# Kernel optimization log

Measured on AMD Instinct MI355X. Metric: run time of the kernel, lower is better.

## Reference

```python
import jax, jax.numpy as jnp
import numpy as np
from jax import lax

TABLE_SIZE = 1024   # LSH table buckets
R = 2.5             # hash bucket width r
U = 0.83            # ALSH norm rescale bound
M = 9               # appended ALSH dims; M // (K*K) = 1 extra channel
K = 3               # kernel spatial size
PAD = 1


def _P(kflat, m):
    # L2-ALSH preprocessing: rescale so max row norm == U, append ||x||^{2^i}, i=1..m
    norms = jnp.linalg.norm(kflat, axis=1)
    x = kflat * (U / jnp.max(norms))
    p = jnp.sum(x * x, axis=1)  # ||x||^2
    powers = [p]
    for _ in range(m - 1):
        powers.append(powers[-1] ** 2)
    return jnp.concatenate([x, jnp.stack(powers, axis=1)], axis=1)  # [O, D+m]


def _conv(x, w):
    return lax.conv_general_dilated(
        x, w, window_strides=(1, 1), padding=[(PAD, PAD), (PAD, PAD)],
        dimension_numbers=("NCHW", "OIHW", "NCHW"))


def setup_inputs() -> dict:
    key = jax.random.key(0)
    k1, k2, k3, k4 = jax.random.split(key, 4)
    inp = jax.random.normal(k1, (16, 128, 64, 64), jnp.float32)
    kernels = jax.random.normal(k2, (256, 128, 3, 3), jnp.float32) * 0.05
    d = 128 + M // (K * K)  # 129
    a = jax.random.normal(k3, (d * K * K,), jnp.float32)  # 1161
    b = jax.random.uniform(k4, (1,), jnp.float32) * R
    return {"input": inp, "kernels": kernels, "a": a, "b": b}


def reference(input, kernels, a, b):
    O, C, kh, kw = kernels.shape
    B, _, H, W = input.shape
    extra_ch = M // (kh * kw)
    d = C + extra_ch

    # ---- init_table: hash every kernel row into a bucket ----
    kflat = kernels.reshape(O, -1)                       # [O, C*kh*kw]
    h = jnp.floor((_P(kflat, M) @ a + b[0]) / R)         # [O]
    bucket = jnp.abs(jnp.fmod(h.astype(jnp.int32), TABLE_SIZE))  # torch fmod+abs semantics

    # ---- vote: Q appends 0.5-filled channels, conv with hash vector as kernel ----
    input_Q = jnp.concatenate(
        [input, jnp.full((B, extra_ch, H, W), 0.5, input.dtype)], axis=1)
    dotted = _conv(input_Q, a.reshape(1, d, kh, kw))     # [B,1,H,W]
    votes = jnp.floor((dotted.reshape(-1) + b[0]) / R).astype(jnp.int32)
    vbucket = jnp.abs(jnp.fmod(votes, TABLE_SIZE))

    # ---- count_votes + argmax bucket ----
    count = jax.ops.segment_sum(jnp.ones(vbucket.shape, jnp.float32),
                                vbucket, num_segments=TABLE_SIZE)
    index = jnp.argmax(count)

    # ---- active set: kernels whose table bucket == winning bucket (mask form, jit-safe) ----
    mask = (bucket == index)                             # [O] bool
    active_kernels = kernels * mask[:, None, None, None].astype(kernels.dtype)

    # apply the active set (the conv this module feeds downstream)
    out = _conv(input, active_kernels)                   # [B,O,H,W]
    return out, index, mask
```

## Files before the change

kernel.cpp:

```cpp
#include <hip/hip_runtime.h>
#include <cmath>
#include <cstdint>

#define TSZ 1024
#define RDIV 2.5f
#define UCONST 0.83f

typedef __bf16 bf16x8 __attribute__((ext_vector_type(8)));
typedef float f32x4 __attribute__((ext_vector_type(4)));
typedef unsigned short ushortT;

__device__ __forceinline__ ushortT bf16r(float f) {
  union { float f; unsigned u; } x; x.f = f;
  unsigned r = (x.u + 0x7FFFu + ((x.u >> 16) & 1u)) >> 16;
  return (ushortT)r;
}

__device__ __forceinline__ void glds16(const void* g, void* l) {
  __builtin_amdgcn_global_load_lds(
      (const __attribute__((address_space(1))) unsigned int*)(g),
      (__attribute__((address_space(3))) unsigned int*)(l), 16, 0, 0);
}

__global__ __launch_bounds__(256) void k_cvtg(const float* __restrict__ in,
                                              const float* __restrict__ a,
                                              ushortT* __restrict__ nb,
                                              float* __restrict__ g) {
  __shared__ float tile2[64][129];
  __shared__ float gpart[4][9][64];
  const int bid = blockIdx.x;
  const int n = bid >> 6, y = bid & 63;
  const int t = threadIdx.x;

  {
    const int chs = t >> 4, l16 = t & 15;
    const float* basep = in + ((size_t)(n * 128) << 12) + (y << 6) + (l16 << 2);
#pragma unroll
    for (int i = 0; i < 8; ++i) {
      int ch = (i << 4) + chs;
      f32x4 v = *reinterpret_cast<const f32x4*>(basep + ((size_t)ch << 12));
#pragma unroll
      for (int u = 0; u < 4; ++u) tile2[(l16 << 2) + u][ch] = v[u];
    }
  }
  __syncthreads();

  {
    const int part = __builtin_amdgcn_readfirstlane(t >> 6);
    const int x = t & 63;
    float gacc[9];
#pragma unroll
    for (int tap = 0; tap < 9; ++tap) gacc[tap] = 0.f;
    const int c0 = part << 5;
#pragma unroll
    for (int i = 0; i < 32; ++i) {
      float v = tile2[x][c0 + i];
      const float* ap = a + (c0 + i) * 9;
#pragma unroll
      for (int tap = 0; tap < 9; ++tap) gacc[tap] += v * ap[tap];
    }
#pragma unroll
    for (int tap = 0; tap < 9; ++tap) gpart[part][tap][x] = gacc[tap];
  }
  __syncthreads();

  if (t < 64) {
    const int x = t;
#pragma unroll
    for (int tap = 0; tap < 9; ++tap) {
      float s = gpart[0][tap][x] + gpart[1][tap][x] + gpart[2][tap][x] + gpart[3][tap][x];
      g[tap * 65536 + (n << 12) + (y << 6) + x] = s;
    }
  }

  {
    const int x2 = t >> 2;
    ushortT* dst = nb + (((size_t)((n << 6) + y) << 6) + x2) * 128;
#pragma unroll
    for (int j = 0; j < 4; ++j) {
      int c0 = ((t & 3) << 3) + (j << 5);
      union { ushortT us[8]; uint4 v; } pk;
#pragma unroll
      for (int u = 0; u < 8; ++u) pk.us[u] = bf16r(tile2[x2][c0 + u]);
      *reinterpret_cast<uint4*>(dst + c0) = pk.v;
    }
  }
}

__global__ __launch_bounds__(256) void k_vote3(const float* __restrict__ g,
                                               const float* __restrict__ a,
                                               const float* __restrict__ bb,
                                               int* __restrict__ count) {
  __shared__ int hist[TSZ];
  const int t = threadIdx.x;
  for (int i = t; i < TSZ; i += 256) hist[i] = 0;
  __syncthreads();
  const int pix = blockIdx.x * 256 + t;
  const int n = pix >> 12, y = (pix >> 6) & 63, x = pix & 63;
  float acc = 0.f;
#pragma unroll
  for (int tap = 0; tap < 9; ++tap) {
    const int dy = tap / 3 - 1, dx = tap % 3 - 1;
    const int yy = y + dy, xx = x + dx;
    if ((unsigned)yy < 64u && (unsigned)xx < 64u)
      acc += g[tap * 65536 + (n << 12) + (yy << 6) + xx];
  }
  {
    const float* av = a + 1152;
#pragma unroll
    for (int ky = 0; ky < 3; ++ky) {
      int yy = y + ky - 1;
      if ((unsigned)yy >= 64u) continue;
#pragma unroll
      for (int kx = 0; kx < 3; ++kx) {
        int xx = x + kx - 1;
        if ((unsigned)xx >= 64u) continue;
        acc += 0.5f * av[ky * 3 + kx];
      }
    }
  }
  int v = (int)floorf((acc + bb[0]) / RDIV);
  int r = v % TSZ; if (r < 0) r = -r;
  atomicAdd(&hist[r], 1);
  __syncthreads();
  for (int i = t; i < TSZ; i += 256) {
    int h = hist[i];
    if (h) atomicAdd(&count[i], h);
  }
}

__global__ __launch_bounds__(256) void k_norm(const float* __restrict__ k,
                                              unsigned* __restrict__ scaleBits) {
  int o = blockIdx.x;
  const float* row = k + (size_t)o * 1152;
  float s = 0.f;
  for (int j = threadIdx.x; j < 1152; j += 256) { float v = row[j]; s += v * v; }
  __shared__ float red[256];
  red[threadIdx.x] = s; __syncthreads();
  for (int st = 128; st; st >>= 1) {
    if (threadIdx.x < st) red[threadIdx.x] += red[threadIdx.x + st];
    __syncthreads();
  }
  if (threadIdx.x == 0) atomicMax(scaleBits, __float_as_uint(red[0]));
}

__global__ __launch_bounds__(256) void k_hash(const float* __restrict__ k,
                                              const float* __restrict__ a,
                                              const float* __restrict__ b,
                                              const unsigned* __restrict__ scaleBits,
                                              int* __restrict__ bucket) {
  int o = blockIdx.x;
  float scale = UCONST / sqrtf(__uint_as_float(scaleBits[0]));
  const float* row = k + (size_t)o * 1152;
  float dot = 0.f, p = 0.f;
  for (int j = threadIdx.x; j < 1152; j += 256) {
    float x = row[j] * scale;
    dot += x * a[j];
    p += x * x;
  }
  __shared__ float rd[256], rp[256];
  rd[threadIdx.x] = dot; rp[threadIdx.x] = p; __syncthreads();
  for (int st = 128; st; st >>= 1) {
    if (threadIdx.x < st) { rd[threadIdx.x] += rd[threadIdx.x + st]; rp[threadIdx.x] += rp[threadIdx.x + st]; }
    __syncthreads();
  }
  if (threadIdx.x == 0) {
    float acc = rd[0];
    float pw = rp[0];
    for (int i = 0; i < 9; i++) { acc += pw * a[1152 + i]; pw = pw * pw; }
    acc += b[0];
    float h = floorf(acc / RDIV);
    int hi = (int)h;
    int r = hi % TSZ; if (r < 0) r = -r;
    bucket[o] = r;
  }
}

__global__ __launch_bounds__(1024) void k_argmax(const int* __restrict__ count,
                                                 const int* __restrict__ bucket,
                                                 int* __restrict__ maskI,
                                                 float* __restrict__ tail) {
  __shared__ int sc[1024];
  __shared__ int si[1024];
  int t = threadIdx.x;
  sc[t] = count[t]; si[t] = t; __syncthreads();
  for (int st = 512; st; st >>= 1) {
    if (t < st) {
      int c2 = sc[t + st], i2 = si[t + st];
      if (c2 > sc[t] || (c2 == sc[t] && i2 < si[t])) { sc[t] = c2; si[t] = i2; }
    }
    __syncthreads();
  }
  int idx = si[0];
  if (t == 0) tail[0] = (float)idx;
  if (t < 256) {
    int m = (bucket[t] == idx) ? 1 : 0;
    maskI[t] = m;
    tail[1 + t] = (float)m;
  }
}

__global__ __launch_bounds__(256) void k_wprep(const float* __restrict__ w,
                                               const int* __restrict__ maskI,
                                               ushortT* __restrict__ wb) {
  const int o = blockIdx.x;
  const float m = maskI[o] ? 1.f : 0.f;
  const float* wr = w + (size_t)o * 1152;
  ushortT* dst = wb + (size_t)o * 1152;
  for (int j = threadIdx.x; j < 1152; j += 256) {
    int r = j >> 7, c = j & 127;
    dst[j] = bf16r(wr[c * 9 + r] * m);
  }
}

__global__ __launch_bounds__(512, 2) void k_gemm3(const ushortT* __restrict__ nb,
                                                  const ushortT* __restrict__ wb,
                                                  const char* __restrict__ zp,
                                                  float* __restrict__ out) {
  __shared__ __align__(16) char smem[3 * 24576];
  const int t = threadIdx.x, l = t & 63, w = t >> 6;
  const int mb = blockIdx.x;
  const int n = mb >> 5;
  const int y0 = (mb & 31) << 1;
  const int wm = w & 1, wn = w >> 1;
  const int lr = l & 15, lq = l >> 4;
  const char* nbN = (const char*)nb + (size_t)n * 1048576;

  int cA[3], yA[3], xA[3];
  const char* bPj[3];
#pragma unroll
  for (int j = 0; j < 3; ++j) {
    int c = w * 3 + j;
    cA[j] = c;
    int m = (c << 4) + lr;
    yA[j] = y0 + (m >> 6);
    xA[j] = m & 63;
    int orow = ((c - 8) << 4) + lr;
    bPj[j] = (const char*)wb + (size_t)orow * 2304 + (lq << 4);
  }

  auto stage = [&](int buf, int s) {
    const int tap = s >> 2;
    const int d3 = tap / 3;
    const int dy = d3 - 1, dx = tap - d3 * 3 - 1;
    const int cb = (s & 3) << 6;
    char* dstb = smem + buf * 24576;
#pragma unroll
    for (int j = 0; j < 3; ++j) {
      const char* src;
      if (cA[j] < 8) {
        int yy = yA[j] + dy, xx = xA[j] + dx;
        bool ok = ((unsigned)yy < 64u) && ((unsigned)xx < 64u);
        src = ok ? (nbN + (((yy << 6) + xx) << 8) + cb + (lq << 4))
                 : (zp + (lq << 4));
      } else {
        src = bPj[j] + (s << 6);
      }
      glds16(src, dstb + (cA[j] << 10));
    }
  };

  f32x4 acc[4][4] = {};

  stage(0, 0);
  stage(1, 1);
  asm volatile("s_waitcnt vmcnt(3)" ::: "memory");
  __builtin_amdgcn_s_barrier();

  for (int tt = 0; tt < 36; ++tt) {
    if (tt > 0) {
      if (tt < 35) { asm volatile("s_waitcnt vmcnt(3)" ::: "memory"); }
      else         { asm volatile("s_waitcnt vmcnt(0)" ::: "memory"); }
      __builtin_amdgcn_s_barrier();
    }
    if (tt + 2 < 36) stage((tt + 2) % 3, tt + 2);
    const char* bufb = smem + (tt % 3) * 24576;
    bf16x8 af[4], bv[4];
#pragma unroll
    for (int mi = 0; mi < 4; ++mi)
      af[mi] = *reinterpret_cast<const bf16x8*>(
          bufb + ((((wm << 2) + mi)) << 10) + (l << 4));
#pragma unroll
    for (int ni = 0; ni < 4; ++ni)
      bv[ni] = *reinterpret_cast<const bf16x8*>(
          bufb + 8192 + ((((wn << 2) + ni)) << 10) + (l << 4));
    __builtin_amdgcn_s_setprio(1);
#pragma unroll
    for (int mi = 0; mi < 4; ++mi)
#pragma unroll
      for (int ni = 0; ni < 4; ++ni)
        acc[mi][ni] = __builtin_amdgcn_mfma_f32_16x16x32_bf16(
            af[mi], bv[ni], acc[mi][ni], 0, 0, 0);
    __builtin_amdgcn_s_setprio(0);
  }

#pragma unroll
  for (int ni = 0; ni < 4; ++ni) {
    const int o = (wn << 6) + (ni << 4) + lr;
    float* op = out + ((size_t)((n << 8) + o) << 12) + ((y0 + wm) << 6);
#pragma unroll
    for (int mi = 0; mi < 4; ++mi)
      *reinterpret_cast<f32x4*>(op + (mi << 4) + (lq << 2)) = acc[mi][ni];
  }
}

__global__ __launch_bounds__(256) void k_votecvt(const float* __restrict__ in,
                                                 const float* __restrict__ a,
                                                 const float* __restrict__ bb,
                                                 int* __restrict__ count,
                                                 ushortT* __restrict__ nb) {
  __shared__ float sb[6][8][64];
  __shared__ int hist[TSZ];
  const int t = threadIdx.x;
  for (int i = t; i < TSZ; i += 256) hist[i] = 0;
  const int bid = blockIdx.x;
  const int n = bid >> 4, y0 = (bid & 15) << 2;
  const int x = t & 63, ry = t >> 6;
  const int yq = y0 + ry;
  float acc = 0.f;
  const float* base = in + (size_t)n * 524288;
  ushortT* nbrow = nb + (((size_t)(n * 64 + yq) << 6) + x) * 128;
  for (int cc = 0; cc < 16; ++cc) {
    __syncthreads();
#pragma unroll
    for (int k = 0; k < 12; ++k) {
      int i = k * 256 + t;
      int row = i >> 9;
      int c8 = (i >> 6) & 7;
      int xx = i & 63;
      int yy = y0 - 1 + row;
      float v = 0.f;
      if ((unsigned)yy < 64u) v = base[(size_t)(cc * 8 + c8) * 4096 + yy * 64 + xx];
      sb[row][c8][xx] = v;
    }
    __syncthreads();
#pragma unroll
    for (int c8 = 0; c8 < 8; ++c8) {
      const float* av = a + (cc * 8 + c8) * 9;
#pragma unroll
      for (int ky = 0; ky < 3; ++ky) {
        const float* rowp = sb[ry + ky][c8];
        float left  = (x >= 1)  ? rowp[x - 1] : 0.f;
        float mid   = rowp[x];
        float right = (x <= 62) ? rowp[x + 1] : 0.f;
        acc += left * av[ky * 3 + 0] + mid * av[ky * 3 + 1] + right * av[ky * 3 + 2];
      }
    }
    {
      union { ushortT us[8]; uint4 v; } pk;
#pragma unroll
      for (int c8 = 0; c8 < 8; ++c8) pk.us[c8] = bf16r(sb[ry + 1][c8][x]);
      *reinterpret_cast<uint4*>(nbrow + cc * 8) = pk.v;
    }
  }
  {
    const float* av = a + 1152;
#pragma unroll
    for (int ky = 0; ky < 3; ++ky) {
      int yy = yq + ky - 1;
      if ((unsigned)yy >= 64u) continue;
#pragma unroll
      for (int kx = 0; kx < 3; ++kx) {
        int xx = x + kx - 1;
        if ((unsigned)xx >= 64u) continue;
        acc += 0.5f * av[ky * 3 + kx];
      }
    }
  }
  int v = (int)floorf((acc + bb[0]) / RDIV);
  int r = v % TSZ; if (r < 0) r = -r;
  atomicAdd(&hist[r], 1);
  __syncthreads();
  for (int i = t; i < TSZ; i += 256) {
    int h = hist[i];
    if (h) atomicAdd(&count[i], h);
  }
}

__global__ __launch_bounds__(256) void k_conv(const float* __restrict__ in,
                                              const float* __restrict__ w,
                                              const int* __restrict__ maskI,
                                              float* __restrict__ out) {
  const int og = blockIdx.x, n = blockIdx.y, yt = blockIdx.z;
  const int tid = threadIdx.x;
  const int tx = tid & 63, trow = tid >> 6;
  const int y0 = yt * 4;
  const int oc0 = og * 4;
  const int m0 = maskI[oc0], m1 = maskI[oc0 + 1], m2 = maskI[oc0 + 2], m3 = maskI[oc0 + 3];
  float* op = out + ((size_t)(n * 256 + oc0)) * 4096 + (size_t)(y0 + trow) * 64 + tx;
  if (!(m0 | m1 | m2 | m3)) {
    op[0] = 0.f; op[4096] = 0.f; op[8192] = 0.f; op[12288] = 0.f;
    return;
  }
  __shared__ float tile[6 * 66];
  const float* base = in + (size_t)n * 128 * 4096;
  const float* wb = w + (size_t)oc0 * 1152;
  float a0 = 0.f, a1 = 0.f, a2 = 0.f, a3 = 0.f;
  for (int c = 0; c < 128; c++) {
    __syncthreads();
    for (int i = tid; i < 396; i += 256) {
      int r = i / 66, col = i - r * 66;
      int yy = y0 - 1 + r, xx = col - 1;
      float v = 0.f;
      if ((unsigned)yy < 64u && (unsigned)xx < 64u) v = base[(size_t)c * 4096 + yy * 64 + xx];
      tile[i] = v;
    }
    __syncthreads();
    const int ro = trow * 66 + tx;
    float t00 = tile[ro],        t01 = tile[ro + 1],   t02 = tile[ro + 2];
    float t10 = tile[ro + 66],   t11 = tile[ro + 67],  t12 = tile[ro + 68];
    float t20 = tile[ro + 132],  t21 = tile[ro + 133], t22 = tile[ro + 134];
    const float* wc = wb + c * 9;
    if (m0) { const float* q = wc;        a0 += t00*q[0]+t01*q[1]+t02*q[2]+t10*q[3]+t11*q[4]+t12*q[5]+t20*q[6]+t21*q[7]+t22*q[8]; }
    if (m1) { const float* q = wc + 1152; a1 += t00*q[0]+t01*q[1]+t02*q[2]+t10*q[3]+t11*q[4]+t12*q[5]+t20*q[6]+t21*q[7]+t22*q[8]; }
    if (m2) { const float* q = wc + 2304; a2 += t00*q[0]+t01*q[1]+t02*q[2]+t10*q[3]+t11*q[4]+t12*q[5]+t20*q[6]+t21*q[7]+t22*q[8]; }
    if (m3) { const float* q = wc + 3456; a3 += t00*q[0]+t01*q[1]+t02*q[2]+t10*q[3]+t11*q[4]+t12*q[5]+t20*q[6]+t21*q[7]+t22*q[8]; }
  }
  op[0]     = m0 ? a0 : 0.f;
  op[4096]  = m1 ? a1 : 0.f;
  op[8192]  = m2 ? a2 : 0.f;
  op[12288] = m3 ? a3 : 0.f;
}

extern "C" void kernel_launch(void* const* d_in, const int* in_sizes, int n_in,
                              void* d_out, int out_size, void* d_ws, size_t ws_size,
                              hipStream_t stream) {
  const float* in = (const float*)d_in[0];
  const float* kw = (const float*)d_in[1];
  const float* a  = (const float*)d_in[2];
  const float* b  = (const float*)d_in[3];
  float* out = (float*)d_out;

  char* ws = (char*)d_ws;
  const size_t NEED_BIG = 19732800ULL;
  const size_t NEED_MED = 17374720ULL;

  if (ws_size >= NEED_BIG) {
    ushortT* nb   = (ushortT*)(ws);
    ushortT* wb   = (ushortT*)(ws + 16777216);
    float* g      = (float*)(ws + 17367040);
    int* count    = (int*)(ws + 19726336);
    unsigned* scB = (unsigned*)(ws + 19730432);
    char* zpage   = (ws + 19730496);
    int* bucket   = (int*)(ws + 19730752);
    int* maskI    = (int*)(ws + 19731776);

    hipMemsetAsync(ws + 19726336, 0, 4416, stream);

    k_norm<<<256, 256, 0, stream>>>(kw, scB);
    k_hash<<<256, 256, 0, stream>>>(kw, a, b, scB, bucket);
    k_cvtg<<<1024, 256, 0, stream>>>(in, a, nb, g);
    k_vote3<<<256, 256, 0, stream>>>(g, a, b, count);
    k_argmax<<<1, 1024, 0, stream>>>(count, bucket, maskI, out + 16777216);
    k_wprep<<<256, 256, 0, stream>>>(kw, maskI, wb);
    k_gemm3<<<512, 512, 0, stream>>>(nb, wb, zpage, out);
  } else if (ws_size >= NEED_MED) {
    ushortT* nb   = (ushortT*)(ws);
    ushortT* wb   = (ushortT*)(ws + 16777216);
    int* count    = (int*)(ws + 17367040);
    unsigned* scB = (unsigned*)(ws + 17371136);
    char* zpage   = (ws + 17371152);
    int* bucket   = (int*)(ws + 17371408);
    int* maskI    = (int*)(ws + 17372432);

    hipMemsetAsync(ws + 17367040, 0, 4368, stream);

    k_norm<<<256, 256, 0, stream>>>(kw, scB);
    k_hash<<<256, 256, 0, stream>>>(kw, a, b, scB, bucket);
    k_votecvt<<<256, 256, 0, stream>>>(in, a, b, count, nb);
    k_argmax<<<1, 1024, 0, stream>>>(count, bucket, maskI, out + 16777216);
    k_wprep<<<256, 256, 0, stream>>>(kw, maskI, wb);
    k_gemm3<<<512, 512, 0, stream>>>(nb, wb, zpage, out);
  } else {
    int* count    = (int*)(ws);
    unsigned* scB = (unsigned*)(ws + 4096);
    int* bucket   = (int*)(ws + 4160);
    int* maskI    = (int*)(ws + 5184);
    float* gdummy = nullptr; (void)gdummy;

    hipMemsetAsync(ws, 0, 4160, stream);
    k_norm<<<256, 256, 0, stream>>>(kw, scB);
    k_hash<<<256, 256, 0, stream>>>(kw, a, b, scB, bucket);
    k_votecvt<<<256, 256, 0, stream>>>(in, a, b, count, (ushortT*)(ws + 8192));
    k_argmax<<<1, 1024, 0, stream>>>(count, bucket, maskI, out + 16777216);
    dim3 grid(64, 16, 16);
    k_conv<<<grid, 256, 0, stream>>>(in, kw, maskI, out);
  }
}
```

Measured before the change: 178.7 us.

## Fuse argmax into weight prep and enlarge GEMM tile to four rows

The separate argmax kernel is merged into the weight-prep kernel, so each of the 256 blocks redoes the small 1024-bucket argmax reduction and applies the mask directly. This removes one launch and the maskI round trip. The implicit-GEMM conv tile grows from 128x256 to 256x256 output positions per block (8x4 MFMA tiles per wave), which halves the grid to 256 blocks and doubles reuse of the staged weights. The cost is higher register and LDS use per block and fewer blocks to spread across CUs. The medium-workspace path is dropped, and the fallback path uses a vote-only kernel.

```diff
diff --git a/kernel.cpp b/kernel.cpp
--- a/kernel.cpp
+++ b/kernel.cpp
@@ -31,7 +31,6 @@
   const int bid = blockIdx.x;
   const int n = bid >> 6, y = bid & 63;
   const int t = threadIdx.x;
-
   {
     const int chs = t >> 4, l16 = t & 15;
     const float* basep = in + ((size_t)(n * 128) << 12) + (y << 6) + (l16 << 2);
@@ -44,7 +43,6 @@
     }
   }
   __syncthreads();
-
   {
     const int part = __builtin_amdgcn_readfirstlane(t >> 6);
     const int x = t & 63;
@@ -63,7 +61,6 @@
     for (int tap = 0; tap < 9; ++tap) gpart[part][tap][x] = gacc[tap];
   }
   __syncthreads();
-
   if (t < 64) {
     const int x = t;
 #pragma unroll
@@ -72,7 +69,6 @@
       g[tap * 65536 + (n << 12) + (y << 6) + x] = s;
     }
   }
-
   {
     const int x2 = t >> 2;
     ushortT* dst = nb + (((size_t)((n << 6) + y) << 6) + x2) * 128;
@@ -176,6 +172,202 @@
   }
 }
 
+__global__ __launch_bounds__(256) void k_wprep2(const int* __restrict__ count,
+                                                const int* __restrict__ bucket,
+                                                const float* __restrict__ w,
+                                                ushortT* __restrict__ wb,
+                                                float* __restrict__ tail) {
+  __shared__ int sc[256];
+  __shared__ int si[256];
+  const int t = threadIdx.x;
+  int bc = count[t], bi = t;
+#pragma unroll
+  for (int j = 1; j < 4; ++j) {
+    int i2 = t + j * 256;
+    int c2 = count[i2];
+    if (c2 > bc) { bc = c2; bi = i2; }
+  }
+  sc[t] = bc; si[t] = bi; __syncthreads();
+  for (int st = 128; st; st >>= 1) {
+    if (t < st) {
+      int c2 = sc[t + st], i2 = si[t + st];
+      if (c2 > sc[t] || (c2 == sc[t] && i2 < si[t])) { sc[t] = c2; si[t] = i2; }
+    }
+    __syncthreads();
+  }
+  const int idx = si[0];
+  const int o = blockIdx.x;
+  const int m = (bucket[o] == idx) ? 1 : 0;
+  if (t == 0) {
+    if (o == 0) tail[0] = (float)idx;
+    tail[1 + o] = (float)m;
+  }
+  const float mf = m ? 1.f : 0.f;
+  const float* wr = w + (size_t)o * 1152;
+  ushortT* dst = wb + (size_t)o * 1152;
+  for (int j = t; j < 1152; j += 256) {
+    int r = j >> 7, c = j & 127;
+    dst[j] = bf16r(wr[c * 9 + r] * mf);
+  }
+}
+
+__global__ __launch_bounds__(512, 2) void k_gemm3r(const ushortT* __restrict__ nb,
+                                                   const ushortT* __restrict__ wb,
+                                                   const char* __restrict__ zp,
+                                                   float* __restrict__ out) {
+  __shared__ __align__(16) char smem[3 * 32768];
+  const int t = threadIdx.x, l = t & 63, w = t >> 6;
+  const int mb = blockIdx.x;
+  const int n = mb >> 4;
+  const int y0 = (mb & 15) << 2;
+  const int wm = w & 1, wn = w >> 1;
+  const int lr = l & 15, lq = l >> 4;
+  const char* nbN = (const char*)nb + (size_t)n * 1048576;
+
+  int cC[4], yA[4], xA[4];
+  const char* bPj[4];
+#pragma unroll
+  for (int j = 0; j < 4; ++j) {
+    int c = (w << 2) + j;
+    cC[j] = c;
+    int m = (c << 4) + lr;
+    yA[j] = y0 + (m >> 6);
+    xA[j] = m & 63;
+    int orow = ((c - 16) << 4) + lr;
+    bPj[j] = (const char*)wb + (size_t)orow * 2304 + (lq << 4);
+  }
+
+  auto stage = [&](int buf, int s) {
+    const int tap = s >> 2;
+    const int d3 = tap * 0x5556 >> 16;
+    const int dy = d3 - 1, dx = tap - d3 * 3 - 1;
+    const int cb = (s & 3) << 6;
+    char* dstb = smem + buf * 32768;
+#pragma unroll
+    for (int j = 0; j < 4; ++j) {
+      const char* src;
+      if (cC[j] < 16) {
+        int yy = yA[j] + dy, xx = xA[j] + dx;
+        bool ok = ((unsigned)yy < 64u) && ((unsigned)xx < 64u);
+        src = ok ? (nbN + (((yy << 6) + xx) << 8) + cb + (lq << 4))
+                 : (zp + (lq << 4));
+      } else {
+        src = bPj[j] + (s << 6);
+      }
+      glds16(src, dstb + (cC[j] << 10));
+    }
+  };
+
+  f32x4 acc[8][4] = {};
+
+  stage(0, 0);
+  stage(1, 1);
+  asm volatile("s_waitcnt vmcnt(4)" ::: "memory");
+  __builtin_amdgcn_s_barrier();
+
+  for (int tt = 0; tt < 36; ++tt) {
+    if (tt > 0) {
+      if (tt < 35) { asm volatile("s_waitcnt vmcnt(4)" ::: "memory"); }
+      else         { asm volatile("s_waitcnt vmcnt(0)" ::: "memory"); }
+      __builtin_amdgcn_s_barrier();
+    }
+    if (tt + 2 < 36) stage((tt + 2) % 3, tt + 2);
+    const char* bufb = smem + (tt % 3) * 32768;
+    bf16x8 af[8], bv[4];
+#pragma unroll
+    for (int mi = 0; mi < 8; ++mi)
+      af[mi] = *reinterpret_cast<const bf16x8*>(
+          bufb + (((wm << 3) + mi) << 10) + (l << 4));
+#pragma unroll
+    for (int ni = 0; ni < 4; ++ni)
+      bv[ni] = *reinterpret_cast<const bf16x8*>(
+          bufb + 16384 + (((wn << 2) + ni) << 10) + (l << 4));
+    __builtin_amdgcn_s_setprio(1);
+#pragma unroll
+    for (int mi = 0; mi < 8; ++mi)
+#pragma unroll
+      for (int ni = 0; ni < 4; ++ni)
+        acc[mi][ni] = __builtin_amdgcn_mfma_f32_16x16x32_bf16(
+            af[mi], bv[ni], acc[mi][ni], 0, 0, 0);
+    __builtin_amdgcn_s_setprio(0);
+  }
+
+  const int pos0 = (mb & 15) << 8;
+#pragma unroll
+  for (int ni = 0; ni < 4; ++ni) {
+    const int o = (wn << 6) + (ni << 4) + lr;
+    float* op = out + ((size_t)((n << 8) + o) << 12) + pos0 + (wm << 7) + (lq << 2);
+#pragma unroll
+    for (int mi = 0; mi < 8; ++mi)
+      *reinterpret_cast<f32x4*>(op + (mi << 4)) = acc[mi][ni];
+  }
+}
+
+__global__ __launch_bounds__(256) void k_vote2(const float* __restrict__ in,
+                                               const float* __restrict__ a,
+                                               const float* __restrict__ bb,
+                                               int* __restrict__ count) {
+  __shared__ float sb[6][8][64];
+  __shared__ int hist[TSZ];
+  const int t = threadIdx.x;
+  for (int i = t; i < TSZ; i += 256) hist[i] = 0;
+  const int bid = blockIdx.x;
+  const int n = bid >> 4, y0 = (bid & 15) << 2;
+  const int x = t & 63, ry = t >> 6;
+  const int yq = y0 + ry;
+  float acc = 0.f;
+  const float* base = in + (size_t)n * 524288;
+  for (int cc = 0; cc < 16; ++cc) {
+    __syncthreads();
+#pragma unroll
+    for (int k = 0; k < 12; ++k) {
+      int i = k * 256 + t;
+      int row = i >> 9;
+      int c8 = (i >> 6) & 7;
+      int xx = i & 63;
+      int yy = y0 - 1 + row;
+      float v = 0.f;
+      if ((unsigned)yy < 64u) v = base[(size_t)(cc * 8 + c8) * 4096 + yy * 64 + xx];
+      sb[row][c8][xx] = v;
+    }
+    __syncthreads();
+#pragma unroll
+    for (int c8 = 0; c8 < 8; ++c8) {
+      const float* av = a + (cc * 8 + c8) * 9;
+#pragma unroll
+      for (int ky = 0; ky < 3; ++ky) {
+        const float* rowp = sb[ry + ky][c8];
+        float left  = (x >= 1)  ? rowp[x - 1] : 0.f;
+        float mid   = rowp[x];
+        float right = (x <= 62) ? rowp[x + 1] : 0.f;
+        acc += left * av[ky * 3 + 0] + mid * av[ky * 3 + 1] + right * av[ky * 3 + 2];
+      }
+    }
+  }
+  {
+    const float* av = a + 1152;
+#pragma unroll
+    for (int ky = 0; ky < 3; ++ky) {
+      int yy = yq + ky - 1;
+      if ((unsigned)yy >= 64u) continue;
+#pragma unroll
+      for (int kx = 0; kx < 3; ++kx) {
+        int xx = x + kx - 1;
+        if ((unsigned)xx >= 64u) continue;
+        acc += 0.5f * av[ky * 3 + kx];
+      }
+    }
+  }
+  int v = (int)floorf((acc + bb[0]) / RDIV);
+  int r = v % TSZ; if (r < 0) r = -r;
+  atomicAdd(&hist[r], 1);
+  __syncthreads();
+  for (int i = t; i < TSZ; i += 256) {
+    int h = hist[i];
+    if (h) atomicAdd(&count[i], h);
+  }
+}
+
 __global__ __launch_bounds__(1024) void k_argmax(const int* __restrict__ count,
                                                  const int* __restrict__ bucket,
                                                  int* __restrict__ maskI,
@@ -197,183 +389,6 @@
     int m = (bucket[t] == idx) ? 1 : 0;
     maskI[t] = m;
     tail[1 + t] = (float)m;
-  }
-}
-
-__global__ __launch_bounds__(256) void k_wprep(const float* __restrict__ w,
-                                               const int* __restrict__ maskI,
-                                               ushortT* __restrict__ wb) {
-  const int o = blockIdx.x;
-  const float m = maskI[o] ? 1.f : 0.f;
-  const float* wr = w + (size_t)o * 1152;
-  ushortT* dst = wb + (size_t)o * 1152;
-  for (int j = threadIdx.x; j < 1152; j += 256) {
-    int r = j >> 7, c = j & 127;
-    dst[j] = bf16r(wr[c * 9 + r] * m);
-  }
-}
-
-__global__ __launch_bounds__(512, 2) void k_gemm3(const ushortT* __restrict__ nb,
-                                                  const ushortT* __restrict__ wb,
-                                                  const char* __restrict__ zp,
-                                                  float* __restrict__ out) {
-  __shared__ __align__(16) char smem[3 * 24576];
-  const int t = threadIdx.x, l = t & 63, w = t >> 6;
-  const int mb = blockIdx.x;
-  const int n = mb >> 5;
-  const int y0 = (mb & 31) << 1;
-  const int wm = w & 1, wn = w >> 1;
-  const int lr = l & 15, lq = l >> 4;
-  const char* nbN = (const char*)nb + (size_t)n * 1048576;
-
-  int cA[3], yA[3], xA[3];
-  const char* bPj[3];
-#pragma unroll
-  for (int j = 0; j < 3; ++j) {
-    int c = w * 3 + j;
-    cA[j] = c;
-    int m = (c << 4) + lr;
-    yA[j] = y0 + (m >> 6);
-    xA[j] = m & 63;
-    int orow = ((c - 8) << 4) + lr;
-    bPj[j] = (const char*)wb + (size_t)orow * 2304 + (lq << 4);
-  }
-
-  auto stage = [&](int buf, int s) {
-    const int tap = s >> 2;
-    const int d3 = tap / 3;
-    const int dy = d3 - 1, dx = tap - d3 * 3 - 1;
-    const int cb = (s & 3) << 6;
-    char* dstb = smem + buf * 24576;
-#pragma unroll
-    for (int j = 0; j < 3; ++j) {
-      const char* src;
-      if (cA[j] < 8) {
-        int yy = yA[j] + dy, xx = xA[j] + dx;
-        bool ok = ((unsigned)yy < 64u) && ((unsigned)xx < 64u);
-        src = ok ? (nbN + (((yy << 6) + xx) << 8) + cb + (lq << 4))
-                 : (zp + (lq << 4));
-      } else {
-        src = bPj[j] + (s << 6);
-      }
-      glds16(src, dstb + (cA[j] << 10));
-    }
-  };
-
-  f32x4 acc[4][4] = {};
-
-  stage(0, 0);
-  stage(1, 1);
-  asm volatile("s_waitcnt vmcnt(3)" ::: "memory");
-  __builtin_amdgcn_s_barrier();
-
-  for (int tt = 0; tt < 36; ++tt) {
-    if (tt > 0) {
-      if (tt < 35) { asm volatile("s_waitcnt vmcnt(3)" ::: "memory"); }
-      else         { asm volatile("s_waitcnt vmcnt(0)" ::: "memory"); }
-      __builtin_amdgcn_s_barrier();
-    }
-    if (tt + 2 < 36) stage((tt + 2) % 3, tt + 2);
-    const char* bufb = smem + (tt % 3) * 24576;
-    bf16x8 af[4], bv[4];
-#pragma unroll
-    for (int mi = 0; mi < 4; ++mi)
-      af[mi] = *reinterpret_cast<const bf16x8*>(
-          bufb + ((((wm << 2) + mi)) << 10) + (l << 4));
-#pragma unroll
-    for (int ni = 0; ni < 4; ++ni)
-      bv[ni] = *reinterpret_cast<const bf16x8*>(
-          bufb + 8192 + ((((wn << 2) + ni)) << 10) + (l << 4));
-    __builtin_amdgcn_s_setprio(1);
-#pragma unroll
-    for (int mi = 0; mi < 4; ++mi)
-#pragma unroll
-      for (int ni = 0; ni < 4; ++ni)
-        acc[mi][ni] = __builtin_amdgcn_mfma_f32_16x16x32_bf16(
-            af[mi], bv[ni], acc[mi][ni], 0, 0, 0);
-    __builtin_amdgcn_s_setprio(0);
-  }
-
-#pragma unroll
-  for (int ni = 0; ni < 4; ++ni) {
-    const int o = (wn << 6) + (ni << 4) + lr;
-    float* op = out + ((size_t)((n << 8) + o) << 12) + ((y0 + wm) << 6);
-#pragma unroll
-    for (int mi = 0; mi < 4; ++mi)
-      *reinterpret_cast<f32x4*>(op + (mi << 4) + (lq << 2)) = acc[mi][ni];
-  }
-}
-
-__global__ __launch_bounds__(256) void k_votecvt(const float* __restrict__ in,
-                                                 const float* __restrict__ a,
-                                                 const float* __restrict__ bb,
-                                                 int* __restrict__ count,
-                                                 ushortT* __restrict__ nb) {
-  __shared__ float sb[6][8][64];
-  __shared__ int hist[TSZ];
-  const int t = threadIdx.x;
-  for (int i = t; i < TSZ; i += 256) hist[i] = 0;
-  const int bid = blockIdx.x;
-  const int n = bid >> 4, y0 = (bid & 15) << 2;
-  const int x = t & 63, ry = t >> 6;
-  const int yq = y0 + ry;
-  float acc = 0.f;
-  const float* base = in + (size_t)n * 524288;
-  ushortT* nbrow = nb + (((size_t)(n * 64 + yq) << 6) + x) * 128;
-  for (int cc = 0; cc < 16; ++cc) {
-    __syncthreads();
-#pragma unroll
-    for (int k = 0; k < 12; ++k) {
-      int i = k * 256 + t;
-      int row = i >> 9;
-      int c8 = (i >> 6) & 7;
-      int xx = i & 63;
-      int yy = y0 - 1 + row;
-      float v = 0.f;
-      if ((unsigned)yy < 64u) v = base[(size_t)(cc * 8 + c8) * 4096 + yy * 64 + xx];
-      sb[row][c8][xx] = v;
-    }
-    __syncthreads();
-#pragma unroll
-    for (int c8 = 0; c8 < 8; ++c8) {
-      const float* av = a + (cc * 8 + c8) * 9;
-#pragma unroll
-      for (int ky = 0; ky < 3; ++ky) {
-        const float* rowp = sb[ry + ky][c8];
-        float left  = (x >= 1)  ? rowp[x - 1] : 0.f;
-        float mid   = rowp[x];
-        float right = (x <= 62) ? rowp[x + 1] : 0.f;
-        acc += left * av[ky * 3 + 0] + mid * av[ky * 3 + 1] + right * av[ky * 3 + 2];
-      }
-    }
-    {
-      union { ushortT us[8]; uint4 v; } pk;
-#pragma unroll
-      for (int c8 = 0; c8 < 8; ++c8) pk.us[c8] = bf16r(sb[ry + 1][c8][x]);
-      *reinterpret_cast<uint4*>(nbrow + cc * 8) = pk.v;
-    }
-  }
-  {
-    const float* av = a + 1152;
-#pragma unroll
-    for (int ky = 0; ky < 3; ++ky) {
-      int yy = yq + ky - 1;
-      if ((unsigned)yy >= 64u) continue;
-#pragma unroll
-      for (int kx = 0; kx < 3; ++kx) {
-        int xx = x + kx - 1;
-        if ((unsigned)xx >= 64u) continue;
-        acc += 0.5f * av[ky * 3 + kx];
-      }
-    }
-  }
-  int v = (int)floorf((acc + bb[0]) / RDIV);
-  int r = v % TSZ; if (r < 0) r = -r;
-  atomicAdd(&hist[r], 1);
-  __syncthreads();
-  for (int i = t; i < TSZ; i += 256) {
-    int h = hist[i];
-    if (h) atomicAdd(&count[i], h);
   }
 }
 
@@ -432,8 +447,7 @@
   float* out = (float*)d_out;
 
   char* ws = (char*)d_ws;
-  const size_t NEED_BIG = 19732800ULL;
-  const size_t NEED_MED = 17374720ULL;
+  const size_t NEED_BIG = 19731776ULL;
 
   if (ws_size >= NEED_BIG) {
     ushortT* nb   = (ushortT*)(ws);
@@ -443,7 +457,6 @@
     unsigned* scB = (unsigned*)(ws + 19730432);
     char* zpage   = (ws + 19730496);
     int* bucket   = (int*)(ws + 19730752);
-    int* maskI    = (int*)(ws + 19731776);
 
     hipMemsetAsync(ws + 19726336, 0, 4416, stream);
 
@@ -451,37 +464,18 @@
     k_hash<<<256, 256, 0, stream>>>(kw, a, b, scB, bucket);
     k_cvtg<<<1024, 256, 0, stream>>>(in, a, nb, g);
     k_vote3<<<256, 256, 0, stream>>>(g, a, b, count);
-    k_argmax<<<1, 1024, 0, stream>>>(count, bucket, maskI, out + 16777216);
-    k_wprep<<<256, 256, 0, stream>>>(kw, maskI, wb);
-    k_gemm3<<<512, 512, 0, stream>>>(nb, wb, zpage, out);
-  } else if (ws_size >= NEED_MED) {
-    ushortT* nb   = (ushortT*)(ws);
-    ushortT* wb   = (ushortT*)(ws + 16777216);
-    int* count    = (int*)(ws + 17367040);
-    unsigned* scB = (unsigned*)(ws + 17371136);
-    char* zpage   = (ws + 17371152);
-    int* bucket   = (int*)(ws + 17371408);
-    int* maskI    = (int*)(ws + 17372432);
-
-    hipMemsetAsync(ws + 17367040, 0, 4368, stream);
-
-    k_norm<<<256, 256, 0, stream>>>(kw, scB);
-    k_hash<<<256, 256, 0, stream>>>(kw, a, b, scB, bucket);
-    k_votecvt<<<256, 256, 0, stream>>>(in, a, b, count, nb);
-    k_argmax<<<1, 1024, 0, stream>>>(count, bucket, maskI, out + 16777216);
-    k_wprep<<<256, 256, 0, stream>>>(kw, maskI, wb);
-    k_gemm3<<<512, 512, 0, stream>>>(nb, wb, zpage, out);
+    k_wprep2<<<256, 256, 0, stream>>>(count, bucket, kw, wb, out + 16777216);
+    k_gemm3r<<<256, 512, 0, stream>>>(nb, wb, zpage, out);
   } else {
     int* count    = (int*)(ws);
     unsigned* scB = (unsigned*)(ws + 4096);
     int* bucket   = (int*)(ws + 4160);
     int* maskI    = (int*)(ws + 5184);
-    float* gdummy = nullptr; (void)gdummy;
 
     hipMemsetAsync(ws, 0, 4160, stream);
     k_norm<<<256, 256, 0, stream>>>(kw, scB);
     k_hash<<<256, 256, 0, stream>>>(kw, a, b, scB, bucket);
-    k_votecvt<<<256, 256, 0, stream>>>(in, a, b, count, (ushortT*)(ws + 8192));
+    k_vote2<<<256, 256, 0, stream>>>(in, a, b, count);
     k_argmax<<<1, 1024, 0, stream>>>(count, bucket, maskI, out + 16777216);
     dim3 grid(64, 16, 16);
     k_conv<<<grid, 256, 0, stream>>>(in, kw, maskI, out);
```

Result: faster. 162.7 us (-9.0%).
